# Kernel tuning notes

Hardware: AMD Instinct MI355X
Metric: run time of the kernel (lower is better)

The kernel has to match this reference:

```python
import jax, jax.numpy as jnp
import numpy as np

N, S, D, H = 2048, 16, 128, 8
EPS = 1e-5  # torch.nn.LayerNorm default eps


def setup_inputs() -> dict:
    key = jax.random.key(0)
    ks = jax.random.split(key, 3)
    return {
        "x": jax.random.normal(ks[0], (N, S, D), jnp.float32),
        "Wi": jax.random.normal(ks[1], (H, S, D, D), jnp.float32),
        "Wj": jax.random.normal(ks[2], (H, S, 2 * D, D), jnp.float32),
        "ln1_w": jnp.ones((S, D), jnp.float32),
        "ln1_b": jnp.zeros((S, D), jnp.float32),
        "prelu1_a": jnp.float32(0.25),  # torch PReLU default single param
        "ln2_w": jnp.ones((H, D), jnp.float32),
        "ln2_b": jnp.zeros((H, D), jnp.float32),
        "prelu2_a": jnp.float32(0.25),
    }


def _layernorm2(x, w, b):
    # LayerNorm over the last two dims (matches torch LayerNorm([A, B]))
    mu = jnp.mean(x, axis=(-2, -1), keepdims=True)
    var = jnp.var(x, axis=(-2, -1), keepdims=True)
    return (x - mu) * jax.lax.rsqrt(var + EPS) * w + b


def _prelu(x, a):
    return jnp.where(x >= 0, x, a * x)


def reference(x, Wi, Wj, ln1_w, ln1_b, prelu1_a, ln2_w, ln2_b, prelu2_a):
    n, s, d = x.shape
    h = Wi.shape[0]
    # sort descending along source dim
    idx = jnp.argsort(-x, axis=1)                      # [N,S,D] int
    x_sort = jnp.take_along_axis(x, idx, axis=1)       # [N,S,D]
    # pad with a zero row, take adjacent differences
    pad = jnp.concatenate([x_sort, jnp.zeros((n, 1, d), x.dtype)], axis=1)
    diff = pad[:, :-1, :] - pad[:, 1:, :]              # [N,S,D]
    # positional encoding: cumsum of 2^rank / 2^S
    enc = jnp.cumsum(jnp.exp2(idx.astype(x.dtype)), axis=1) / jnp.asarray(2.0 ** s, x.dtype)
    # per-head, per-source batched matmul with Wi
    se = jnp.einsum('bsd,hsdo->bhso', enc, Wi)         # [N,H,S,D]
    se = _prelu(_layernorm2(se, ln1_w, ln1_b), prelu1_a)  # Dropout in eval mode = identity
    cat = jnp.concatenate(
        [jnp.broadcast_to(diff[:, None, :, :], (n, h, s, d)), se], axis=-1
    )                                                  # [N,H,S,2D]
    out = jnp.einsum('bhsd,hsdo->bho', cat, Wj)        # [N,H,D]
    return _prelu(_layernorm2(out, ln2_w, ln2_b), prelu2_a)
```

## Files before the change

kernel.cpp:

```cpp
#include <hip/hip_runtime.h>

#define N_ 2048
#define S_ 16
#define D_ 128
#define H_ 8
#define EPS_ 1e-5f

typedef unsigned short ushortT;
typedef unsigned int uint32;
typedef __attribute__((ext_vector_type(8))) short short8;
typedef __attribute__((ext_vector_type(8))) unsigned short ushort8;
typedef __attribute__((ext_vector_type(4))) float f32x4;
typedef __attribute__((ext_vector_type(4))) unsigned int uint4v;
typedef __attribute__((ext_vector_type(8))) float float8;

__device__ __forceinline__ ushortT f2bf(float f) {
  union { float f; uint32 u; } c; c.f = f;
  uint32 u = c.u;
  u = (u + 0x7FFFu + ((u >> 16) & 1u)) >> 16;
  return (ushortT)u;
}
__device__ __forceinline__ float bf2f(ushortT b) {
  union { uint32 u; float f; } c; c.u = ((uint32)b) << 16;
  return c.f;
}

__global__ __launch_bounds__(256) void k_prep(const float* __restrict__ x,
                                              ushortT* __restrict__ enc,
                                              ushortT* __restrict__ diff_sw) {
  int g = blockIdx.x * 256 + threadIdx.x;
  int n = g >> 7, d = g & 127;
  const float* xp = x + (size_t)n * (S_ * D_) + d;
  float v[S_];
#pragma unroll
  for (int s = 0; s < S_; ++s) v[s] = xp[s * D_];
  int r[S_];
#pragma unroll
  for (int i = 0; i < S_; ++i) {
    int ri = 0;
#pragma unroll
    for (int j = 0; j < S_; ++j)
      ri += ((v[j] > v[i]) || (v[j] == v[i] && j < i)) ? 1 : 0;
    r[i] = ri;
  }
  float xs[S_ + 1];
#pragma unroll
  for (int s = 0; s < S_; ++s) {
    float acc = 0.f;
#pragma unroll
    for (int i = 0; i < S_; ++i) acc += (r[i] == s) ? v[i] : 0.f;
    xs[s] = acc;
  }
  xs[S_] = 0.f;
  ushortT* ep = enc + (size_t)n * (S_ * D_) + d;
  int btq = n >> 7, rr = n & 127, pp = d >> 6, c8p = (d >> 3) & 7, ee = d & 7;
  int q = rr * 8 + (c8p ^ (rr & 7));
#pragma unroll
  for (int s = 0; s < S_; ++s) {
    uint32 mm = 0;
#pragma unroll
    for (int i = 0; i < S_; ++i) mm |= (r[i] <= s) ? (1u << i) : 0u;
    ep[s * D_] = f2bf((float)mm * (1.f / 65536.f));
    size_t idx = ((((size_t)(btq * 16 + s) * 2 + pp) * 1024) + q) * 8 + ee;
    diff_sw[idx] = f2bf(xs[s] - xs[s + 1]);
  }
}

__global__ __launch_bounds__(256) void k_castW(const float* __restrict__ Wi,
                                               const float* __restrict__ Wj,
                                               ushortT* __restrict__ Wit,
                                               ushortT* __restrict__ Wjt_sw) {
  __shared__ ushortT tile[128 * 136];
  int bx = blockIdx.x;
  int t = threadIdx.x;
  if (bx < 128) {
    int hs = bx;
    const float* src = Wi + (size_t)hs * D_ * D_;
#pragma unroll 4
    for (int i = 0; i < 64; ++i) {
      int e = t + 256 * i;
      int dd = e >> 7, o = e & 127;
      tile[dd * 136 + o] = f2bf(src[e]);
    }
    __syncthreads();
    int o = t >> 1, dbase = (t & 1) * 64;
    ushortT* dst = Wit + ((size_t)hs * D_ + o) * D_ + dbase;
#pragma unroll
    for (int c = 0; c < 8; ++c) {
      uint4v pk;
#pragma unroll
      for (int q = 0; q < 4; ++q) {
        ushortT lo = tile[(dbase + c * 8 + q * 2) * 136 + o];
        ushortT hi = tile[(dbase + c * 8 + q * 2 + 1) * 136 + o];
        pk[q] = (uint32)lo | ((uint32)hi << 16);
      }
      *(uint4v*)(dst + c * 8) = pk;
    }
  } else {
    int hs = bx - 128; int h = hs >> 4, s = hs & 15;
    const float* src = Wj + (size_t)hs * 256 * D_;
    for (int half = 0; half < 2; ++half) {
      if (half) __syncthreads();
#pragma unroll 4
      for (int i = 0; i < 64; ++i) {
        int e = t + 256 * i;
        int dd = e >> 7, o = e & 127;
        tile[dd * 136 + o] = f2bf(src[half * 16384 + e]);
      }
      __syncthreads();
      int o = t >> 1, db = (t & 1) * 64;
      int part = half * 2 + (t & 1);
      ushortT* dst = Wjt_sw + ((size_t)(h * 16 + s) * 4 + part) * 8192;
#pragma unroll
      for (int c = 0; c < 8; ++c) {
        uint4v pk;
#pragma unroll
        for (int q = 0; q < 4; ++q) {
          ushortT lo = tile[(db + c * 8 + q * 2) * 136 + o];
          ushortT hi = tile[(db + c * 8 + q * 2 + 1) * 136 + o];
          pk[q] = (uint32)lo | ((uint32)hi << 16);
        }
        *(uint4v*)(dst + (o * 8 + (c ^ (o & 7))) * 8) = pk;
      }
    }
  }
}

__global__ __launch_bounds__(256) void k_gemm1(const ushortT* __restrict__ enc,
                                               const ushortT* __restrict__ Wit,
                                               ushortT* __restrict__ se,
                                               float* __restrict__ ssum,
                                               float* __restrict__ ssq) {
  int bt = blockIdx.x, s = blockIdx.y, hp = blockIdx.z;
  int h0 = hp * 4;
  __shared__ ushortT As[128 * 128];
  __shared__ ushortT Bs[128 * 128];
  int tid = threadIdx.x;
  int c16 = tid & 15, prow = tid >> 4;
  int wave = tid >> 6, lane = tid & 63;
  int l15 = lane & 15, lg = lane >> 4;

  ushort8 rb[8];
#pragma unroll
  for (int i = 0; i < 8; ++i) {
    int row = prow + 16 * i;
    int sw = ((c16 ^ (row & 7)) * 8);
    ushort8 va = *(const ushort8*)(enc + (size_t)(bt * 128 + row) * (S_ * D_) + s * D_ + c16 * 8);
    *(ushort8*)(As + row * 128 + sw) = va;
    rb[i] = *(const ushort8*)(Wit + ((size_t)((h0 * S_ + s) * D_) + row) * D_ + c16 * 8);
  }
  __syncthreads();
  short8 afr[4][2];
#pragma unroll
  for (int kk = 0; kk < 4; ++kk)
#pragma unroll
    for (int i = 0; i < 2; ++i) {
      int row = wave * 32 + i * 16 + l15;
      int cc = kk * 4 + lg;
      afr[kk][i] = *(const short8*)(As + row * 128 + ((cc ^ (row & 7)) * 8));
    }

  for (int hh = 0; hh < 4; ++hh) {
    int h = h0 + hh;
    if (hh) __syncthreads();
#pragma unroll
    for (int i = 0; i < 8; ++i) {
      int row = prow + 16 * i;
      *(ushort8*)(Bs + row * 128 + ((c16 ^ (row & 7)) * 8)) = rb[i];
    }
    if (hh < 3) {
#pragma unroll
      for (int i = 0; i < 8; ++i) {
        int row = prow + 16 * i;
        rb[i] = *(const ushort8*)(Wit + ((size_t)(((h + 1) * S_ + s) * D_) + row) * D_ + c16 * 8);
      }
    }
    __syncthreads();
    f32x4 acc[2][8];
#pragma unroll
    for (int i = 0; i < 2; ++i)
#pragma unroll
      for (int j = 0; j < 8; ++j) acc[i][j] = (f32x4)(0.f);
#pragma unroll
    for (int kk = 0; kk < 4; ++kk) {
      int cc = kk * 4 + lg;
      short8 b[8];
#pragma unroll
      for (int j = 0; j < 8; ++j) {
        int row = j * 16 + l15;
        b[j] = *(const short8*)(Bs + row * 128 + ((cc ^ (row & 7)) * 8));
      }
#pragma unroll
      for (int i = 0; i < 2; ++i)
#pragma unroll
        for (int j = 0; j < 8; ++j)
          acc[i][j] = __builtin_amdgcn_mfma_f32_16x16x32_bf16(afr[kk][i], b[j], acc[i][j], 0, 0, 0);
    }
#pragma unroll
    for (int i = 0; i < 2; ++i)
#pragma unroll
      for (int rr = 0; rr < 4; ++rr) {
        int rloc = wave * 32 + i * 16 + lg * 4 + rr;
        int b_g = bt * 128 + rloc;
        float rs = 0.f, rq = 0.f;
#pragma unroll
        for (int j = 0; j < 8; ++j) {
          float val = acc[i][j][rr];
          rs += val; rq += val * val;
        }
#pragma unroll
        for (int m = 1; m <= 8; m <<= 1) {
          rs += __shfl_xor(rs, m);
          rq += __shfl_xor(rq, m);
        }
        if (l15 == 0) {
          ssum[((size_t)s * N_ + b_g) * H_ + h] = rs;
          ssq[((size_t)s * N_ + b_g) * H_ + h] = rq;
        }
      }
    __syncthreads();
#pragma unroll
    for (int i = 0; i < 2; ++i)
#pragma unroll
      for (int rr = 0; rr < 4; ++rr) {
        int row = wave * 32 + i * 16 + lg * 4 + rr;
        int sw = (row & 7) << 3;
#pragma unroll
        for (int j = 0; j < 8; ++j) {
          int o = j * 16 + l15;
          Bs[row * 128 + (o ^ sw)] = f2bf(acc[i][j][rr]);
        }
      }
    __syncthreads();
#pragma unroll
    for (int p = 0; p < 2; ++p) {
      int row = p * 64 + (tid >> 2);
      int sw = (row & 7) << 3;
      int b_g = bt * 128 + row;
      ushortT* dst = se + (((size_t)b_g * H_ + h) * S_ + s) * D_;
#pragma unroll
      for (int q = 0; q < 4; ++q) {
        int o0 = (q * 4 + (tid & 3)) * 8;
        *(uint4v*)(dst + o0) = *(const uint4v*)(Bs + row * 128 + (o0 ^ sw));
      }
    }
  }
}

__global__ __launch_bounds__(256) void k_finalize(const float* __restrict__ ssum,
                                                  const float* __restrict__ ssq,
                                                  float* __restrict__ mr) {
  int t = blockIdx.x * 256 + threadIdx.x;
  float s1 = 0.f, s2 = 0.f;
#pragma unroll
  for (int s = 0; s < S_; ++s) {
    s1 += ssum[(size_t)s * (N_ * H_) + t];
    s2 += ssq[(size_t)s * (N_ * H_) + t];
  }
  float mu = s1 * (1.f / 2048.f);
  float var = s2 * (1.f / 2048.f) - mu * mu;
  float rstd = rsqrtf(var + EPS_);
  mr[t * 2] = rstd;
  mr[t * 2 + 1] = -mu * rstd;
}

#define GLDS_TILE(DST, SRC) do {                                              \
    const ushortT* sp_ = (SRC) + wave * 512 + lane * 8;                       \
    ushortT* dp_ = (DST) + wave * 512;                                        \
    _Pragma("unroll")                                                         \
    for (int i_ = 0; i_ < 4; ++i_)                                            \
      __builtin_amdgcn_global_load_lds(                                       \
          (const __attribute__((address_space(1))) void*)(sp_ + i_ * 2048),   \
          (__attribute__((address_space(3))) void*)(dp_ + i_ * 2048),         \
          16, 0, 0);                                                          \
  } while (0)

__global__ __launch_bounds__(256, 2) void k_gemm2(const ushortT* __restrict__ diff_sw,
                                                  const ushortT* __restrict__ se,
                                                  const ushortT* __restrict__ Wjt_sw,
                                                  const float* __restrict__ mr,
                                                  const float* __restrict__ ln1w,
                                                  const float* __restrict__ ln1b,
                                                  const float* __restrict__ pa1,
                                                  float* __restrict__ outp,
                                                  int scount) {
  int bt = blockIdx.x, sh = blockIdx.y, h = blockIdx.z;
  int s0 = sh * scount;
  __shared__ ushortT As[2][128 * 64];
  __shared__ ushortT Bs[2][128 * 64];
  int tid = threadIdx.x;
  int wave = tid >> 6, lane = tid & 63;
  int c8 = tid & 7, trow = tid >> 3;
  int swst = ((c8 ^ (trow & 7)) * 8);
  int l15 = lane & 15, lg = lane >> 4;
  int wm = wave >> 1, wn = wave & 1;
  float a1 = pa1[0];

  float rs_r[4], nm_r[4];
  uint32 aoff_s[4];
#pragma unroll
  for (int i = 0; i < 4; ++i) {
    int row = i * 32 + trow;
    int b_g = bt * 128 + row;
    rs_r[i] = mr[((size_t)b_g * H_ + h) * 2];
    nm_r[i] = mr[((size_t)b_g * H_ + h) * 2 + 1];
    aoff_s[i] = ((uint32)b_g * H_ + h) * (S_ * D_) + c8 * 8;
  }
  ushort8 raL[4], raH[4];
  f32x4 acc[4][4];
#pragma unroll
  for (int i = 0; i < 4; ++i)
#pragma unroll
    for (int j = 0; j < 4; ++j) acc[i][j] = (f32x4)(0.f);

#define COMPUTE(XBUF) do {                                                    \
    _Pragma("unroll")                                                         \
    for (int kk = 0; kk < 2; ++kk) {                                          \
      int cc = kk * 4 + lg;                                                   \
      short8 a[4], b[4];                                                      \
      _Pragma("unroll")                                                       \
      for (int i = 0; i < 4; ++i) {                                           \
        int row = wm * 64 + i * 16 + l15;                                     \
        a[i] = *(const short8*)(As[XBUF] + row * 64 + ((cc ^ (row & 7)) * 8));\
      }                                                                       \
      _Pragma("unroll")                                                       \
      for (int j = 0; j < 4; ++j) {                                           \
        int row = wn * 64 + j * 16 + l15;                                     \
        b[j] = *(const short8*)(Bs[XBUF] + row * 64 + ((cc ^ (row & 7)) * 8));\
      }                                                                       \
      _Pragma("unroll")                                                       \
      for (int i = 0; i < 4; ++i)                                             \
        _Pragma("unroll")                                                     \
        for (int j = 0; j < 4; ++j)                                           \
          acc[i][j] = __builtin_amdgcn_mfma_f32_16x16x32_bf16(a[i], b[j],     \
                                                              acc[i][j], 0, 0, 0); \
    } } while (0)

#define TRANSFORM_WRITE(RA, NXBUF, SS, HALF) do {                             \
    float8 w8 = *(const float8*)(ln1w + (SS) * D_ + (HALF) * 64 + c8 * 8);    \
    float8 b8 = *(const float8*)(ln1b + (SS) * D_ + (HALF) * 64 + c8 * 8);    \
    _Pragma("unroll")                                                         \
    for (int i = 0; i < 4; ++i) {                                             \
      int row = i * 32 + trow;                                                \
      float y[8];                                                             \
      _Pragma("unroll")                                                       \
      for (int e = 0; e < 8; ++e) {                                           \
        float f = bf2f((ushortT)RA[i][e]);                                    \
        float tt = fmaf(f, rs_r[i], nm_r[i]);                                 \
        float vv = fmaf(tt, w8[e], b8[e]);                                    \
        y[e] = fmaf(a1, fminf(vv, 0.f), fmaxf(vv, 0.f));                      \
      }                                                                       \
      uint4v pk;                                                              \
      _Pragma("unroll")                                                       \
      for (int q = 0; q < 4; ++q) {                                           \
        uint32 rpk;                                                           \
        asm("v_cvt_pk_bf16_f32 %0, %1, %2" : "=v"(rpk)                        \
            : "v"(y[2 * q]), "v"(y[2 * q + 1]));                              \
        pk[q] = rpk;                                                          \
      }                                                                       \
      *(uint4v*)(As[NXBUF] + row * 64 + swst) = pk;                           \
    } } while (0)

  GLDS_TILE(As[0], diff_sw + ((size_t)(bt * 16 + s0) * 2 + 0) * 8192);
  GLDS_TILE(Bs[0], Wjt_sw + ((size_t)(h * 16 + s0) * 4 + 0) * 8192);
  __syncthreads();

  for (int si = 0; si < scount; ++si) {
    int s = s0 + si;
    int sn = (s + 1 < S_) ? s + 1 : 0;
#pragma unroll
    for (int i = 0; i < 4; ++i)
      raL[i] = *(const ushort8*)(se + aoff_s[i] + s * D_);
    GLDS_TILE(As[1], diff_sw + ((size_t)(bt * 16 + s) * 2 + 1) * 8192);
    GLDS_TILE(Bs[1], Wjt_sw + ((size_t)(h * 16 + s) * 4 + 1) * 8192);
    COMPUTE(0);
    __syncthreads();
#pragma unroll
    for (int i = 0; i < 4; ++i)
      raH[i] = *(const ushort8*)(se + aoff_s[i] + s * D_ + 64);
    TRANSFORM_WRITE(raL, 0, s, 0);
    GLDS_TILE(Bs[0], Wjt_sw + ((size_t)(h * 16 + s) * 4 + 2) * 8192);
    COMPUTE(1);
    __syncthreads();
    TRANSFORM_WRITE(raH, 1, s, 1);
    GLDS_TILE(Bs[1], Wjt_sw + ((size_t)(h * 16 + s) * 4 + 3) * 8192);
    COMPUTE(0);
    __syncthreads();
    GLDS_TILE(As[0], diff_sw + ((size_t)(bt * 16 + sn) * 2 + 0) * 8192);
    GLDS_TILE(Bs[0], Wjt_sw + ((size_t)(h * 16 + sn) * 4 + 0) * 8192);
    COMPUTE(1);
    __syncthreads();
  }

#pragma unroll
  for (int i = 0; i < 4; ++i)
#pragma unroll
    for (int j = 0; j < 4; ++j)
#pragma unroll
      for (int rr = 0; rr < 4; ++rr) {
        int b_g = bt * 128 + wm * 64 + i * 16 + lg * 4 + rr;
        int o = wn * 64 + j * 16 + l15;
        outp[(((size_t)sh * N_ + b_g) * H_ + h) * D_ + o] = acc[i][j][rr];
      }
}

__global__ __launch_bounds__(256) void k_ln2(const float* __restrict__ outp,
                                             const float* __restrict__ ln2w,
                                             const float* __restrict__ ln2b,
                                             const float* __restrict__ pa2,
                                             float* __restrict__ out,
                                             int nsplit) {
  int b = blockIdx.x, t = threadIdx.x;
  __shared__ float red[8];
  __shared__ float stats[2];
  f32x4 v = (f32x4)(0.f);
  for (int p = 0; p < nsplit; ++p)
    v += *((const f32x4*)(outp + (size_t)p * (N_ * 1024) + (size_t)b * 1024) + t);
  float s1 = v[0] + v[1] + v[2] + v[3];
  float s2 = v[0] * v[0] + v[1] * v[1] + v[2] * v[2] + v[3] * v[3];
#pragma unroll
  for (int m = 1; m <= 32; m <<= 1) {
    s1 += __shfl_xor(s1, m);
    s2 += __shfl_xor(s2, m);
  }
  int wave = t >> 6, lane = t & 63;
  if (lane == 0) { red[wave] = s1; red[4 + wave] = s2; }
  __syncthreads();
  if (t == 0) {
    float S = red[0] + red[1] + red[2] + red[3];
    float Q = red[4] + red[5] + red[6] + red[7];
    float mu = S * (1.f / 1024.f);
    float var = Q * (1.f / 1024.f) - mu * mu;
    stats[0] = mu; stats[1] = rsqrtf(var + EPS_);
  }
  __syncthreads();
  float mu = stats[0], rstd = stats[1];
  float a2 = pa2[0];
  f32x4 wv = *((const f32x4*)ln2w + t);
  f32x4 bv = *((const f32x4*)ln2b + t);
  f32x4 r;
#pragma unroll
  for (int e = 0; e < 4; ++e) {
    float y = (v[e] - mu) * rstd * wv[e] + bv[e];
    r[e] = (y >= 0.f) ? y : a2 * y;
  }
  *((f32x4*)(out + (size_t)b * 1024) + t) = r;
}

extern "C" void kernel_launch(void* const* d_in, const int* in_sizes, int n_in,
                              void* d_out, int out_size, void* d_ws, size_t ws_size,
                              hipStream_t stream) {
  const float* x    = (const float*)d_in[0];
  const float* Wi   = (const float*)d_in[1];
  const float* Wj   = (const float*)d_in[2];
  const float* ln1w = (const float*)d_in[3];
  const float* ln1b = (const float*)d_in[4];
  const float* pa1  = (const float*)d_in[5];
  const float* ln2w = (const float*)d_in[6];
  const float* ln2b = (const float*)d_in[7];
  const float* pa2  = (const float*)d_in[8];
  char* ws = (char*)d_ws;
  ushortT* se      = (ushortT*)(ws + 0);
  ushortT* diff_sw = (ushortT*)(ws + 67108864);
  ushortT* Wjt_sw  = (ushortT*)(ws + 75497472);
  float*   outp    = (float*)(ws + 83886080);
  ushortT* enc     = (ushortT*)(ws + 83886080);
  ushortT* Wit     = (ushortT*)(ws + 92274688);
  float*   ssum    = (float*)(ws + 96468992);
  float*   ssq     = (float*)(ws + 97517568);
  float*   out     = (float*)d_out;

  int nsplit = (ws_size >= 117571584ull) ? 4 : 2;
  int scount = S_ / nsplit;
  float* mr = (float*)(ws + 83886080 + (size_t)nsplit * 8388608);

  hipLaunchKernelGGL(k_prep, dim3(1024), dim3(256), 0, stream, x, enc, diff_sw);
  hipLaunchKernelGGL(k_castW, dim3(256), dim3(256), 0, stream, Wi, Wj, Wit, Wjt_sw);
  hipLaunchKernelGGL(k_gemm1, dim3(16, 16, 2), dim3(256), 0, stream, enc, Wit, se, ssum, ssq);
  hipLaunchKernelGGL(k_finalize, dim3(64), dim3(256), 0, stream, ssum, ssq, mr);
  hipLaunchKernelGGL(k_gemm2, dim3(16, nsplit, 8), dim3(256), 0, stream, diff_sw, se, Wjt_sw, mr,
                     ln1w, ln1b, pa1, outp, scount);
  hipLaunchKernelGGL(k_ln2, dim3(2048), dim3(256), 0, stream, outp, ln2w, ln2b, pa2, out, nsplit);
}
```

Baseline: 196.1 us.

## Pre-swizzle enc and Wi into MFMA layouts and split gemm1 per head

k_prep now writes the encoding directly in the per-wave MFMA fragment order, and k_castW writes Wi transposed in the XOR-swizzled LDS image. k_gemm1 can then read A fragments straight from global memory and copy B into LDS with global_load_lds, without register staging. Each block now handles one head instead of looping over four, giving a 16x16x8 grid with a smaller padded LDS tile and a launch bound of 3 blocks per CU. The aim is more parallelism and fewer LDS round trips and barriers. The cost is that each block reloads its A fragments per head, and the Wjt swizzle write order is restructured along the way.

```diff
diff --git a/kernel.cpp b/kernel.cpp
--- a/kernel.cpp
+++ b/kernel.cpp
@@ -26,7 +26,7 @@
 }
 
 __global__ __launch_bounds__(256) void k_prep(const float* __restrict__ x,
-                                              ushortT* __restrict__ enc,
+                                              ushortT* __restrict__ enc_sw,
                                               ushortT* __restrict__ diff_sw) {
   int g = blockIdx.x * 256 + threadIdx.x;
   int n = g >> 7, d = g & 127;
@@ -52,15 +52,19 @@
     xs[s] = acc;
   }
   xs[S_] = 0.f;
-  ushortT* ep = enc + (size_t)n * (S_ * D_) + d;
-  int btq = n >> 7, rr = n & 127, pp = d >> 6, c8p = (d >> 3) & 7, ee = d & 7;
-  int q = rr * 8 + (c8p ^ (rr & 7));
+  int btq = n >> 7, row = n & 127;
+  int wv = row >> 5, ii = (row >> 4) & 1, l = row & 15;
+  int kkm = d >> 5, lgm = (d >> 3) & 3, em = d & 7;
+  int off_nd = (((kkm * 2 + ii) * 64) + (lgm * 16 + l)) * 8 + em;
+  int pp = d >> 6, c8p = (d >> 3) & 7, ee = d & 7;
+  int q = row * 8 + (c8p ^ (row & 7));
 #pragma unroll
   for (int s = 0; s < S_; ++s) {
     uint32 mm = 0;
 #pragma unroll
     for (int i = 0; i < S_; ++i) mm |= (r[i] <= s) ? (1u << i) : 0u;
-    ep[s * D_] = f2bf((float)mm * (1.f / 65536.f));
+    enc_sw[(size_t)((btq * 16 + s) * 4 + wv) * 4096 + off_nd] =
+        f2bf((float)mm * (1.f / 65536.f));
     size_t idx = ((((size_t)(btq * 16 + s) * 2 + pp) * 1024) + q) * 8 + ee;
     diff_sw[idx] = f2bf(xs[s] - xs[s + 1]);
   }
@@ -68,7 +72,7 @@
 
 __global__ __launch_bounds__(256) void k_castW(const float* __restrict__ Wi,
                                                const float* __restrict__ Wj,
-                                               ushortT* __restrict__ Wit,
+                                               ushortT* __restrict__ Wit_sw,
                                                ushortT* __restrict__ Wjt_sw) {
   __shared__ ushortT tile[128 * 136];
   int bx = blockIdx.x;
@@ -83,21 +87,24 @@
       tile[dd * 136 + o] = f2bf(src[e]);
     }
     __syncthreads();
-    int o = t >> 1, dbase = (t & 1) * 64;
-    ushortT* dst = Wit + ((size_t)hs * D_ + o) * D_ + dbase;
-#pragma unroll
-    for (int c = 0; c < 8; ++c) {
+    ushortT* dst = Wit_sw + (size_t)hs * 16384;
+#pragma unroll
+    for (int r8 = 0; r8 < 8; ++r8) {
+      int qc = r8 * 256 + t;
+      int o = qc >> 4;
+      int cc = (qc & 15) ^ (o & 7);
       uint4v pk;
 #pragma unroll
-      for (int q = 0; q < 4; ++q) {
-        ushortT lo = tile[(dbase + c * 8 + q * 2) * 136 + o];
-        ushortT hi = tile[(dbase + c * 8 + q * 2 + 1) * 136 + o];
-        pk[q] = (uint32)lo | ((uint32)hi << 16);
-      }
-      *(uint4v*)(dst + c * 8) = pk;
+      for (int w = 0; w < 4; ++w) {
+        int d0 = cc * 8 + w * 2;
+        ushortT lo = tile[d0 * 136 + o];
+        ushortT hi = tile[(d0 + 1) * 136 + o];
+        pk[w] = (uint32)lo | ((uint32)hi << 16);
+      }
+      *(uint4v*)(dst + qc * 8) = pk;
     }
   } else {
-    int hs = bx - 128; int h = hs >> 4, s = hs & 15;
+    int hs = bx - 128;
     const float* src = Wj + (size_t)hs * 256 * D_;
     for (int half = 0; half < 2; ++half) {
       if (half) __syncthreads();
@@ -108,141 +115,123 @@
         tile[dd * 136 + o] = f2bf(src[half * 16384 + e]);
       }
       __syncthreads();
-      int o = t >> 1, db = (t & 1) * 64;
-      int part = half * 2 + (t & 1);
-      ushortT* dst = Wjt_sw + ((size_t)(h * 16 + s) * 4 + part) * 8192;
-#pragma unroll
-      for (int c = 0; c < 8; ++c) {
+      ushortT* dstb = Wjt_sw + ((size_t)hs * 4 + half * 2) * 8192;
+#pragma unroll
+      for (int r8 = 0; r8 < 8; ++r8) {
+        int cg = r8 * 256 + t;
+        int pl = cg >> 10;
+        int qc = cg & 1023;
+        int o = qc >> 3;
+        int c8 = (qc & 7) ^ (o & 7);
+        int dl = pl * 64 + c8 * 8;
         uint4v pk;
 #pragma unroll
-        for (int q = 0; q < 4; ++q) {
-          ushortT lo = tile[(db + c * 8 + q * 2) * 136 + o];
-          ushortT hi = tile[(db + c * 8 + q * 2 + 1) * 136 + o];
-          pk[q] = (uint32)lo | ((uint32)hi << 16);
+        for (int w = 0; w < 4; ++w) {
+          ushortT lo = tile[(dl + w * 2) * 136 + o];
+          ushortT hi = tile[(dl + w * 2 + 1) * 136 + o];
+          pk[w] = (uint32)lo | ((uint32)hi << 16);
         }
-        *(uint4v*)(dst + (o * 8 + (c ^ (o & 7))) * 8) = pk;
-      }
-    }
-  }
-}
-
-__global__ __launch_bounds__(256) void k_gemm1(const ushortT* __restrict__ enc,
-                                               const ushortT* __restrict__ Wit,
-                                               ushortT* __restrict__ se,
-                                               float* __restrict__ ssum,
-                                               float* __restrict__ ssq) {
-  int bt = blockIdx.x, s = blockIdx.y, hp = blockIdx.z;
-  int h0 = hp * 4;
-  __shared__ ushortT As[128 * 128];
-  __shared__ ushortT Bs[128 * 128];
+        *(uint4v*)(dstb + (size_t)pl * 8192 + qc * 8) = pk;
+      }
+    }
+  }
+}
+
+__global__ __launch_bounds__(256, 3) void k_gemm1(const ushortT* __restrict__ enc_sw,
+                                                  const ushortT* __restrict__ Wit_sw,
+                                                  ushortT* __restrict__ se,
+                                                  float* __restrict__ ssum,
+                                                  float* __restrict__ ssq) {
+  int bt = blockIdx.x, s = blockIdx.y, h = blockIdx.z;
+  __shared__ ushortT Bs[128 * 132];
   int tid = threadIdx.x;
-  int c16 = tid & 15, prow = tid >> 4;
   int wave = tid >> 6, lane = tid & 63;
   int l15 = lane & 15, lg = lane >> 4;
 
-  ushort8 rb[8];
-#pragma unroll
-  for (int i = 0; i < 8; ++i) {
-    int row = prow + 16 * i;
-    int sw = ((c16 ^ (row & 7)) * 8);
-    ushort8 va = *(const ushort8*)(enc + (size_t)(bt * 128 + row) * (S_ * D_) + s * D_ + c16 * 8);
-    *(ushort8*)(As + row * 128 + sw) = va;
-    rb[i] = *(const ushort8*)(Wit + ((size_t)((h0 * S_ + s) * D_) + row) * D_ + c16 * 8);
-  }
-  __syncthreads();
+  const ushortT* bsrc = Wit_sw + (size_t)(h * 16 + s) * 16384;
+#pragma unroll
+  for (int r8 = 0; r8 < 8; ++r8)
+    __builtin_amdgcn_global_load_lds(
+        (const __attribute__((address_space(1))) void*)(bsrc + (r8 * 256 + tid) * 8),
+        (__attribute__((address_space(3))) void*)(Bs + (r8 * 256 + wave * 64) * 8),
+        16, 0, 0);
+
   short8 afr[4][2];
+  const ushortT* abase = enc_sw + ((size_t)(bt * 16 + s) * 4 + wave) * 4096;
 #pragma unroll
   for (int kk = 0; kk < 4; ++kk)
 #pragma unroll
-    for (int i = 0; i < 2; ++i) {
-      int row = wave * 32 + i * 16 + l15;
-      int cc = kk * 4 + lg;
-      afr[kk][i] = *(const short8*)(As + row * 128 + ((cc ^ (row & 7)) * 8));
-    }
-
-  for (int hh = 0; hh < 4; ++hh) {
-    int h = h0 + hh;
-    if (hh) __syncthreads();
-#pragma unroll
-    for (int i = 0; i < 8; ++i) {
-      int row = prow + 16 * i;
-      *(ushort8*)(Bs + row * 128 + ((c16 ^ (row & 7)) * 8)) = rb[i];
-    }
-    if (hh < 3) {
-#pragma unroll
-      for (int i = 0; i < 8; ++i) {
-        int row = prow + 16 * i;
-        rb[i] = *(const ushort8*)(Wit + ((size_t)(((h + 1) * S_ + s) * D_) + row) * D_ + c16 * 8);
-      }
-    }
-    __syncthreads();
-    f32x4 acc[2][8];
-#pragma unroll
     for (int i = 0; i < 2; ++i)
-#pragma unroll
-      for (int j = 0; j < 8; ++j) acc[i][j] = (f32x4)(0.f);
-#pragma unroll
-    for (int kk = 0; kk < 4; ++kk) {
-      int cc = kk * 4 + lg;
-      short8 b[8];
+      afr[kk][i] = *(const short8*)(abase + ((kk * 2 + i) * 64 + lane) * 8);
+
+  __syncthreads();
+
+  f32x4 acc[2][8];
+#pragma unroll
+  for (int i = 0; i < 2; ++i)
+#pragma unroll
+    for (int j = 0; j < 8; ++j) acc[i][j] = (f32x4)(0.f);
+#pragma unroll
+  for (int kk = 0; kk < 4; ++kk) {
+    int cc = kk * 4 + lg;
+    short8 b[8];
+#pragma unroll
+    for (int j = 0; j < 8; ++j) {
+      int row = j * 16 + l15;
+      b[j] = *(const short8*)(Bs + (row * 16 + (cc ^ (row & 7))) * 8);
+    }
+#pragma unroll
+    for (int i = 0; i < 2; ++i)
+#pragma unroll
+      for (int j = 0; j < 8; ++j)
+        acc[i][j] = __builtin_amdgcn_mfma_f32_16x16x32_bf16(afr[kk][i], b[j], acc[i][j], 0, 0, 0);
+  }
+#pragma unroll
+  for (int i = 0; i < 2; ++i)
+#pragma unroll
+    for (int rr = 0; rr < 4; ++rr) {
+      int rloc = wave * 32 + i * 16 + lg * 4 + rr;
+      int b_g = bt * 128 + rloc;
+      float rs = 0.f, rq = 0.f;
 #pragma unroll
       for (int j = 0; j < 8; ++j) {
-        int row = j * 16 + l15;
-        b[j] = *(const short8*)(Bs + row * 128 + ((cc ^ (row & 7)) * 8));
-      }
-#pragma unroll
-      for (int i = 0; i < 2; ++i)
-#pragma unroll
-        for (int j = 0; j < 8; ++j)
-          acc[i][j] = __builtin_amdgcn_mfma_f32_16x16x32_bf16(afr[kk][i], b[j], acc[i][j], 0, 0, 0);
-    }
-#pragma unroll
-    for (int i = 0; i < 2; ++i)
-#pragma unroll
-      for (int rr = 0; rr < 4; ++rr) {
-        int rloc = wave * 32 + i * 16 + lg * 4 + rr;
-        int b_g = bt * 128 + rloc;
-        float rs = 0.f, rq = 0.f;
-#pragma unroll
-        for (int j = 0; j < 8; ++j) {
-          float val = acc[i][j][rr];
-          rs += val; rq += val * val;
-        }
-#pragma unroll
-        for (int m = 1; m <= 8; m <<= 1) {
-          rs += __shfl_xor(rs, m);
-          rq += __shfl_xor(rq, m);
-        }
-        if (l15 == 0) {
-          ssum[((size_t)s * N_ + b_g) * H_ + h] = rs;
-          ssq[((size_t)s * N_ + b_g) * H_ + h] = rq;
-        }
-      }
-    __syncthreads();
-#pragma unroll
-    for (int i = 0; i < 2; ++i)
-#pragma unroll
-      for (int rr = 0; rr < 4; ++rr) {
-        int row = wave * 32 + i * 16 + lg * 4 + rr;
-        int sw = (row & 7) << 3;
-#pragma unroll
-        for (int j = 0; j < 8; ++j) {
-          int o = j * 16 + l15;
-          Bs[row * 128 + (o ^ sw)] = f2bf(acc[i][j][rr]);
-        }
-      }
-    __syncthreads();
-#pragma unroll
-    for (int p = 0; p < 2; ++p) {
-      int row = p * 64 + (tid >> 2);
+        float val = acc[i][j][rr];
+        rs += val; rq += val * val;
+      }
+#pragma unroll
+      for (int m = 1; m <= 8; m <<= 1) {
+        rs += __shfl_xor(rs, m);
+        rq += __shfl_xor(rq, m);
+      }
+      if (l15 == 0) {
+        ssum[((size_t)s * N_ + b_g) * H_ + h] = rs;
+        ssq[((size_t)s * N_ + b_g) * H_ + h] = rq;
+      }
+    }
+  __syncthreads();
+#pragma unroll
+  for (int i = 0; i < 2; ++i)
+#pragma unroll
+    for (int rr = 0; rr < 4; ++rr) {
+      int row = wave * 32 + i * 16 + lg * 4 + rr;
       int sw = (row & 7) << 3;
-      int b_g = bt * 128 + row;
-      ushortT* dst = se + (((size_t)b_g * H_ + h) * S_ + s) * D_;
-#pragma unroll
-      for (int q = 0; q < 4; ++q) {
-        int o0 = (q * 4 + (tid & 3)) * 8;
-        *(uint4v*)(dst + o0) = *(const uint4v*)(Bs + row * 128 + (o0 ^ sw));
-      }
+#pragma unroll
+      for (int j = 0; j < 8; ++j) {
+        int o = j * 16 + l15;
+        Bs[row * 132 + (o ^ sw)] = f2bf(acc[i][j][rr]);
+      }
+    }
+  __syncthreads();
+#pragma unroll
+  for (int p = 0; p < 2; ++p) {
+    int row = p * 64 + (tid >> 2);
+    int sw = (row & 7) << 3;
+    int b_g = bt * 128 + row;
+    ushortT* dst = se + (((size_t)b_g * H_ + h) * S_ + s) * D_;
+#pragma unroll
+    for (int qq = 0; qq < 4; ++qq) {
+      int o0 = (qq * 4 + (tid & 3)) * 8;
+      *(uint4v*)(dst + o0) = *(const uint4v*)(Bs + row * 132 + (o0 ^ sw));
     }
   }
 }
@@ -464,8 +453,8 @@
   ushortT* diff_sw = (ushortT*)(ws + 67108864);
   ushortT* Wjt_sw  = (ushortT*)(ws + 75497472);
   float*   outp    = (float*)(ws + 83886080);
-  ushortT* enc     = (ushortT*)(ws + 83886080);
-  ushortT* Wit     = (ushortT*)(ws + 92274688);
+  ushortT* enc_sw  = (ushortT*)(ws + 83886080);
+  ushortT* Wit_sw  = (ushortT*)(ws + 92274688);
   float*   ssum    = (float*)(ws + 96468992);
   float*   ssq     = (float*)(ws + 97517568);
   float*   out     = (float*)d_out;
@@ -474,9 +463,9 @@
   int scount = S_ / nsplit;
   float* mr = (float*)(ws + 83886080 + (size_t)nsplit * 8388608);
 
-  hipLaunchKernelGGL(k_prep, dim3(1024), dim3(256), 0, stream, x, enc, diff_sw);
-  hipLaunchKernelGGL(k_castW, dim3(256), dim3(256), 0, stream, Wi, Wj, Wit, Wjt_sw);
-  hipLaunchKernelGGL(k_gemm1, dim3(16, 16, 2), dim3(256), 0, stream, enc, Wit, se, ssum, ssq);
+  hipLaunchKernelGGL(k_prep, dim3(1024), dim3(256), 0, stream, x, enc_sw, diff_sw);
+  hipLaunchKernelGGL(k_castW, dim3(256), dim3(256), 0, stream, Wi, Wj, Wit_sw, Wjt_sw);
+  hipLaunchKernelGGL(k_gemm1, dim3(16, 16, 8), dim3(256), 0, stream, enc_sw, Wit_sw, se, ssum, ssq);
   hipLaunchKernelGGL(k_finalize, dim3(64), dim3(256), 0, stream, ssum, ssq, mr);
   hipLaunchKernelGGL(k_gemm2, dim3(16, nsplit, 8), dim3(256), 0, stream, diff_sw, se, Wjt_sw, mr,
                      ln1w, ln1b, pa1, outp, scount);
```

New measurement: 188.4 us. 1.04x faster.
